# Performance work log

Hardware: AMD Instinct MI355X
Metric: run time of the kernel (lower is better)

Reference implementation:

```python
import jax, jax.numpy as jnp
import numpy as np

N_NODES = 50000
IN_CH, HID, OUT_CH = 512, 128, 64
N_EDGES = 800000


def gcn_conv(x, edge_index, W, b, num_nodes):
    # PyG GCNConv: add self-loops, symmetric deg^{-1/2} normalization,
    # linear transform then scatter-add aggregation at target nodes.
    row, col = edge_index[0], edge_index[1]
    loop = jnp.arange(num_nodes, dtype=row.dtype)
    rows = jnp.concatenate([row, loop])  # sources
    cols = jnp.concatenate([col, loop])  # targets
    deg = jax.ops.segment_sum(jnp.ones_like(cols, dtype=x.dtype), cols, num_segments=num_nodes)
    dinv = jnp.where(deg > 0, jax.lax.rsqrt(deg), 0.0)
    norm = dinv[rows] * dinv[cols]  # [E+N]
    h = x @ W  # [N, out]
    msg = norm[:, None] * h[rows]  # gather + scale
    out = jax.ops.segment_sum(msg, cols, num_segments=num_nodes)
    return out + b


def setup_inputs() -> dict:
    key = jax.random.key(0)
    k = jax.random.split(key, 8)
    x = jax.random.normal(k[0], (N_NODES, IN_CH), dtype=jnp.float32)
    pos_edge_index = jax.random.randint(k[1], (2, N_EDGES), 0, N_NODES, dtype=jnp.int64 if jax.config.jax_enable_x64 else jnp.int32)
    neg_edge_index = jax.random.randint(k[2], (2, N_EDGES), 0, N_NODES, dtype=pos_edge_index.dtype)
    # Glorot-ish init for weights, zeros for bias (PyG default)
    W1 = jax.random.normal(k[3], (IN_CH, HID), dtype=jnp.float32) * (1.0 / np.sqrt(IN_CH))
    b1 = jnp.zeros((HID,), dtype=jnp.float32)
    W2 = jax.random.normal(k[4], (HID, OUT_CH), dtype=jnp.float32) * (1.0 / np.sqrt(HID))
    b2 = jnp.zeros((OUT_CH,), dtype=jnp.float32)
    return {"x": x, "pos_edge_index": pos_edge_index, "neg_edge_index": neg_edge_index,
            "W1": W1, "b1": b1, "W2": W2, "b2": b2}


def reference(x, pos_edge_index, neg_edge_index, W1, b1, W2, b2):
    n = x.shape[0]
    h = gcn_conv(x, pos_edge_index, W1, b1, n)
    h = jax.nn.relu(h)
    z = gcn_conv(h, pos_edge_index, W2, b2, n)  # encode
    edge_index = jnp.concatenate([pos_edge_index, neg_edge_index], axis=-1)
    # decode: per-edge dot product of endpoint embeddings
    logits = jnp.sum(z[edge_index[0]] * z[edge_index[1]], axis=-1)
    return logits
```

## Files before the change

### kernel.cpp

```cpp
#include <hip/hip_runtime.h>

#define WAVE 64
#define CAP 64

typedef __bf16 v8bf __attribute__((ext_vector_type(8)));
typedef __bf16 v4bf __attribute__((ext_vector_type(4)));
typedef __bf16 v2bf __attribute__((ext_vector_type(2)));
typedef float f32x4 __attribute__((ext_vector_type(4)));

__device__ __forceinline__ void async16(void* lds, const void* g) {
    __builtin_amdgcn_global_load_lds((const __attribute__((address_space(1))) void*)g,
                                     (__attribute__((address_space(3))) void*)lds, 16, 0, 0);
}

__device__ __forceinline__ void cvt8(const f32x4& u, const f32x4& v, v8bf& h, v8bf& l) {
    float f[8] = {u.x, u.y, u.z, u.w, v.x, v.y, v.z, v.w};
#pragma unroll
    for (int j = 0; j < 8; ++j) {
        __bf16 hh = (__bf16)f[j];
        h[j] = hh;
        l[j] = (__bf16)(f[j] - (float)hh);
    }
}

__device__ __forceinline__ void cvt8f(const float4& u, const float4& v, v8bf& h, v8bf& l) {
    float f[8] = {u.x, u.y, u.z, u.w, v.x, v.y, v.z, v.w};
#pragma unroll
    for (int j = 0; j < 8; ++j) {
        __bf16 hh = (__bf16)f[j];
        h[j] = hh;
        l[j] = (__bf16)(f[j] - (float)hh);
    }
}

__global__ __launch_bounds__(256) void prep_kernel(const float* __restrict__ W1,
                                                   const float* __restrict__ W2,
                                                   __bf16* __restrict__ Wt1hi,
                                                   __bf16* __restrict__ Wt1lo,
                                                   __bf16* __restrict__ Wt2hi,
                                                   __bf16* __restrict__ Wt2lo) {
    int b = blockIdx.x;
    int tid = threadIdx.x;
    if (b < 256) {
        int idx = b * 256 + tid;
        int k = idx >> 7, n = idx & 127;
        float v = W1[idx];
        __bf16 h = (__bf16)v;
        Wt1hi[n * 512 + k] = h;
        Wt1lo[n * 512 + k] = (__bf16)(v - (float)h);
    } else {
        int idx = (b - 256) * 256 + tid;
        int k = idx >> 6, n = idx & 63;
        float v = W2[idx];
        __bf16 h = (__bf16)v;
        int o = (k >> 5) * (64 * 32) + n * 32 + (k & 31);
        Wt2hi[o] = h;
        Wt2lo[o] = (__bf16)(v - (float)h);
    }
}

__global__ __launch_bounds__(256) void fill_kernel(const int* __restrict__ ei, int E,
                                                   int* __restrict__ cursor,
                                                   unsigned short* __restrict__ srcs) {
    int e = blockIdx.x * 256 + (int)threadIdx.x;
    if (e >= E) return;
    int dst = ei[E + e];
    int src = ei[e];
    int p = atomicAdd(&cursor[dst], 1);
    if (p < CAP) srcs[(size_t)dst * CAP + p] = (unsigned short)src;
}

template <int NC, int KK, bool OBF16>
__global__ __launch_bounds__(256, 3) void gemm_dinv_kernel(
    const float* __restrict__ A, const __bf16* __restrict__ Bhi,
    const __bf16* __restrict__ Blo, void* __restrict__ Cout, int M, int NG,
    const int* __restrict__ cursor, float* __restrict__ dinv) {
    constexpr int BK = 32;
    constexpr int NT = NC / 16;
    constexpr int NIT = KK / BK;
    constexpr int NCH = NC / 16;

    __shared__ __bf16 sB[2][2][NC * BK];

    const int tid = threadIdx.x;

    if (blockIdx.x >= NG) {
        int i = (blockIdx.x - NG) * 256 + tid;
        if (i < M) dinv[i] = rsqrtf((float)cursor[i] + 1.0f);
        return;
    }

    const int lane = tid & 63;
    const int wv = tid >> 6;
    const int ln15 = lane & 15;
    const int quad = lane >> 4;
    const int rowBase = blockIdx.x * 128;

    const int brow = lane >> 2;
    const int bslot = lane & 3;
    auto stageB = [&](int buf, int k0) {
#pragma unroll
        for (int i = 0; i < NCH / 4; ++i) {
            int c = wv * (NCH / 4) + i;
            int row = c * 16 + brow;
            int gk = k0 + ((bslot ^ (row & 3)) << 3);
            async16(&sB[buf][0][c * 512], Bhi + (size_t)row * KK + gk);
            async16(&sB[buf][1][c * 512], Blo + (size_t)row * KK + gk);
        }
    };

    int r0 = rowBase + wv * 32 + ln15;
    int r1 = r0 + 16;
    if (r0 > M - 1) r0 = M - 1;
    if (r1 > M - 1) r1 = M - 1;
    const float* aP0 = A + (size_t)r0 * KK + quad * 8;
    const float* aP1 = A + (size_t)r1 * KK + quad * 8;

    f32x4 acc[2][NT];
#pragma unroll
    for (int rt = 0; rt < 2; ++rt)
#pragma unroll
        for (int t = 0; t < NT; ++t) acc[rt][t] = (f32x4){0.f, 0.f, 0.f, 0.f};

    float4 aR[4];
    aR[0] = *(const float4*)(aP0);
    aR[1] = *(const float4*)(aP0 + 4);
    aR[2] = *(const float4*)(aP1);
    aR[3] = *(const float4*)(aP1 + 4);

    stageB(0, 0);
    __syncthreads();

    int cur = 0;
    for (int ks = 0; ks < NIT; ++ks) {
        if (ks + 1 < NIT) stageB(cur ^ 1, (ks + 1) * BK);

        v8bf ah[2], al[2];
        cvt8f(aR[0], aR[1], ah[0], al[0]);
        cvt8f(aR[2], aR[3], ah[1], al[1]);
        if (ks + 1 < NIT) {
            aP0 += BK;
            aP1 += BK;
            aR[0] = *(const float4*)(aP0);
            aR[1] = *(const float4*)(aP0 + 4);
            aR[2] = *(const float4*)(aP1);
            aR[3] = *(const float4*)(aP1 + 4);
        }

#pragma unroll
        for (int t = 0; t < NT; ++t) {
            int row = t * 16 + ln15;
            int off = row * BK + ((quad ^ (row & 3)) << 3);
            v8bf bh = *(const v8bf*)&sB[cur][0][off];
            v8bf bl = *(const v8bf*)&sB[cur][1][off];
            acc[0][t] = __builtin_amdgcn_mfma_f32_16x16x32_bf16(ah[0], bh, acc[0][t], 0, 0, 0);
            acc[0][t] = __builtin_amdgcn_mfma_f32_16x16x32_bf16(al[0], bh, acc[0][t], 0, 0, 0);
            acc[0][t] = __builtin_amdgcn_mfma_f32_16x16x32_bf16(ah[0], bl, acc[0][t], 0, 0, 0);
            acc[1][t] = __builtin_amdgcn_mfma_f32_16x16x32_bf16(ah[1], bh, acc[1][t], 0, 0, 0);
            acc[1][t] = __builtin_amdgcn_mfma_f32_16x16x32_bf16(al[1], bh, acc[1][t], 0, 0, 0);
            acc[1][t] = __builtin_amdgcn_mfma_f32_16x16x32_bf16(ah[1], bl, acc[1][t], 0, 0, 0);
        }

        __syncthreads();
        cur ^= 1;
    }

#pragma unroll
    for (int rt = 0; rt < 2; ++rt) {
#pragma unroll
        for (int r = 0; r < 4; ++r) {
            int grow = rowBase + wv * 32 + rt * 16 + quad * 4 + r;
            if (grow < M) {
#pragma unroll
                for (int t = 0; t < NT; ++t) {
                    float v = acc[rt][t][r];
                    if (OBF16)
                        ((__bf16*)Cout)[(size_t)grow * NC + t * 16 + ln15] = (__bf16)v;
                    else
                        ((float*)Cout)[(size_t)grow * NC + t * 16 + ln15] = v;
                }
            }
        }
    }
}

__global__ __launch_bounds__(256) void gather1_gemm2_kernel(
    const __bf16* __restrict__ hs, const int* __restrict__ counts,
    const float* __restrict__ dinv, const unsigned short* __restrict__ srcs,
    const float* __restrict__ bias, const __bf16* __restrict__ W2hi,
    const __bf16* __restrict__ W2lo, __bf16* __restrict__ hs2, int N) {
    constexpr int LDO = 132;
    __shared__ float out1[16 * LDO];

    const int tid = threadIdx.x;
    const int lane = tid & 63;
    const int wv = tid >> 6;
    const int base = blockIdx.x * 16;

    for (int i = 0; i < 4; ++i) {
        int slot = wv * 4 + i;
        int node = base + slot;
        float v0 = 0.f, v1 = 0.f;
        int col = 2 * lane;
        if (node < N) {
            int cnt = counts[node];
            if (cnt > CAP) cnt = CAP;
            int beg = node * CAP;
            int end = beg + cnt;
            float dn = rsqrtf((float)cnt + 1.0f);
            float a0, a1;
            {
                v2bf s = *(const v2bf*)&hs[(size_t)node * 128 + col];
                a0 = dn * (float)s[0];
                a1 = dn * (float)s[1];
            }
            int e = beg;
            for (; e + 8 <= end; e += 8) {
                int s0 = srcs[e], s1 = srcs[e + 1], s2 = srcs[e + 2], s3 = srcs[e + 3];
                int s4 = srcs[e + 4], s5 = srcs[e + 5], s6 = srcs[e + 6], s7 = srcs[e + 7];
                float d0 = dinv[s0], d1 = dinv[s1], d2 = dinv[s2], d3 = dinv[s3];
                float d4 = dinv[s4], d5 = dinv[s5], d6 = dinv[s6], d7 = dinv[s7];
                v2bf r0 = *(const v2bf*)&hs[(size_t)s0 * 128 + col];
                v2bf r1 = *(const v2bf*)&hs[(size_t)s1 * 128 + col];
                v2bf r2 = *(const v2bf*)&hs[(size_t)s2 * 128 + col];
                v2bf r3 = *(const v2bf*)&hs[(size_t)s3 * 128 + col];
                v2bf r4 = *(const v2bf*)&hs[(size_t)s4 * 128 + col];
                v2bf r5 = *(const v2bf*)&hs[(size_t)s5 * 128 + col];
                v2bf r6 = *(const v2bf*)&hs[(size_t)s6 * 128 + col];
                v2bf r7 = *(const v2bf*)&hs[(size_t)s7 * 128 + col];
                a0 += d0 * (float)r0[0] + d1 * (float)r1[0] + d2 * (float)r2[0] + d3 * (float)r3[0] +
                      d4 * (float)r4[0] + d5 * (float)r5[0] + d6 * (float)r6[0] + d7 * (float)r7[0];
                a1 += d0 * (float)r0[1] + d1 * (float)r1[1] + d2 * (float)r2[1] + d3 * (float)r3[1] +
                      d4 * (float)r4[1] + d5 * (float)r5[1] + d6 * (float)r6[1] + d7 * (float)r7[1];
            }
            for (; e < end; ++e) {
                int s0 = srcs[e];
                float d0 = dinv[s0];
                v2bf r0 = *(const v2bf*)&hs[(size_t)s0 * 128 + col];
                a0 += d0 * (float)r0[0];
                a1 += d0 * (float)r0[1];
            }
            float2 bv = *(const float2*)&bias[col];
            v0 = fmaxf(dn * a0 + bv.x, 0.f);
            v1 = fmaxf(dn * a1 + bv.y, 0.f);
        }
        *(float2*)&out1[slot * LDO + col] = make_float2(v0, v1);
    }
    __syncthreads();

    const int ln15 = lane & 15;
    const int quad = lane >> 4;
    f32x4 acc = (f32x4){0.f, 0.f, 0.f, 0.f};
#pragma unroll
    for (int kc = 0; kc < 4; ++kc) {
        const float* ap = &out1[ln15 * LDO + kc * 32 + quad * 8];
        f32x4 u = *(const f32x4*)(ap);
        f32x4 v = *(const f32x4*)(ap + 4);
        v8bf ah, al;
        cvt8(u, v, ah, al);
        size_t bo = (size_t)kc * (64 * 32) + (wv * 16 + ln15) * 32 + quad * 8;
        v8bf bh = *(const v8bf*)(W2hi + bo);
        v8bf bl = *(const v8bf*)(W2lo + bo);
        acc = __builtin_amdgcn_mfma_f32_16x16x32_bf16(ah, bh, acc, 0, 0, 0);
        acc = __builtin_amdgcn_mfma_f32_16x16x32_bf16(al, bh, acc, 0, 0, 0);
        acc = __builtin_amdgcn_mfma_f32_16x16x32_bf16(ah, bl, acc, 0, 0, 0);
    }
#pragma unroll
    for (int r = 0; r < 4; ++r) {
        int node = base + quad * 4 + r;
        if (node < N) hs2[(size_t)node * 64 + wv * 16 + ln15] = (__bf16)acc[r];
    }
}

__global__ __launch_bounds__(256) void gather_agg2(const __bf16* __restrict__ hs,
                                                   const int* __restrict__ counts,
                                                   const float* __restrict__ dinv,
                                                   const unsigned short* __restrict__ srcs,
                                                   const float* __restrict__ bias,
                                                   __bf16* __restrict__ outp, int N) {
    int node = blockIdx.x * 4 + (int)(threadIdx.x >> 6);
    if (node >= N) return;
    int lane = threadIdx.x & 63;
    int cnt = counts[node];
    if (cnt > CAP) cnt = CAP;
    int beg = node * CAP;
    int end = beg + cnt;
    float dn = rsqrtf((float)cnt + 1.0f);

    int q = lane >> 4;
    int sl = lane & 15;
    int col = sl * 4;
    float a0 = 0.f, a1 = 0.f, a2 = 0.f, a3 = 0.f;
    if (q == 0) {
        v4bf s = *(const v4bf*)&hs[(size_t)node * 64 + col];
        a0 = dn * (float)s[0]; a1 = dn * (float)s[1];
        a2 = dn * (float)s[2]; a3 = dn * (float)s[3];
    }
    int e = beg + q;
    for (; e + 12 < end; e += 16) {
        int s0 = srcs[e], s1 = srcs[e + 4], s2 = srcs[e + 8], s3 = srcs[e + 12];
        float d0 = dinv[s0], d1 = dinv[s1], d2 = dinv[s2], d3 = dinv[s3];
        v4bf r0 = *(const v4bf*)&hs[(size_t)s0 * 64 + col];
        v4bf r1 = *(const v4bf*)&hs[(size_t)s1 * 64 + col];
        v4bf r2 = *(const v4bf*)&hs[(size_t)s2 * 64 + col];
        v4bf r3 = *(const v4bf*)&hs[(size_t)s3 * 64 + col];
        a0 += d0 * (float)r0[0] + d1 * (float)r1[0] + d2 * (float)r2[0] + d3 * (float)r3[0];
        a1 += d0 * (float)r0[1] + d1 * (float)r1[1] + d2 * (float)r2[1] + d3 * (float)r3[1];
        a2 += d0 * (float)r0[2] + d1 * (float)r1[2] + d2 * (float)r2[2] + d3 * (float)r3[2];
        a3 += d0 * (float)r0[3] + d1 * (float)r1[3] + d2 * (float)r2[3] + d3 * (float)r3[3];
    }
    for (; e < end; e += 4) {
        int s0 = srcs[e];
        float d0 = dinv[s0];
        v4bf r0 = *(const v4bf*)&hs[(size_t)s0 * 64 + col];
        a0 += d0 * (float)r0[0]; a1 += d0 * (float)r0[1];
        a2 += d0 * (float)r0[2]; a3 += d0 * (float)r0[3];
    }
    a0 += __shfl_xor(a0, 16); a0 += __shfl_xor(a0, 32);
    a1 += __shfl_xor(a1, 16); a1 += __shfl_xor(a1, 32);
    a2 += __shfl_xor(a2, 16); a2 += __shfl_xor(a2, 32);
    a3 += __shfl_xor(a3, 16); a3 += __shfl_xor(a3, 32);
    if (q == 0) {
        float4 bv = *(const float4*)&bias[col];
        v4bf o;
        o[0] = (__bf16)(dn * a0 + bv.x);
        o[1] = (__bf16)(dn * a1 + bv.y);
        o[2] = (__bf16)(dn * a2 + bv.z);
        o[3] = (__bf16)(dn * a3 + bv.w);
        *(v4bf*)&outp[(size_t)node * 64 + col] = o;
    }
}

__global__ __launch_bounds__(256) void decode_bf16_kernel(const __bf16* __restrict__ z,
                                                          const int* __restrict__ pos,
                                                          const int* __restrict__ neg, int E,
                                                          float* __restrict__ out) {
    int tid = blockIdx.x * blockDim.x + threadIdx.x;
    int g = tid >> 2;
    int l = tid & 3;
    int total = 2 * E;
    if (g >= total) return;
    int src, dst;
    if (g < E) {
        src = pos[g];
        dst = pos[E + g];
    } else {
        int e = g - E;
        src = neg[e];
        dst = neg[E + e];
    }
    const __bf16* zs = z + (size_t)src * 64 + l * 16;
    const __bf16* zd = z + (size_t)dst * 64 + l * 16;
    v8bf a0 = *(const v8bf*)zs;
    v8bf a1 = *(const v8bf*)(zs + 8);
    v8bf b0 = *(const v8bf*)zd;
    v8bf b1 = *(const v8bf*)(zd + 8);
    float p = 0.f;
#pragma unroll
    for (int j = 0; j < 8; ++j) p += (float)a0[j] * (float)b0[j] + (float)a1[j] * (float)b1[j];
    p += __shfl_xor(p, 1);
    p += __shfl_xor(p, 2);
    if (l == 0) out[g] = p;
}

extern "C" void kernel_launch(void* const* d_in, const int* in_sizes, int n_in, void* d_out,
                              int out_size, void* d_ws, size_t ws_size, hipStream_t stream) {
    const float* x = (const float*)d_in[0];
    const int* pos_ei = (const int*)d_in[1];
    const int* neg_ei = (const int*)d_in[2];
    const float* W1 = (const float*)d_in[3];
    const float* b1 = (const float*)d_in[4];
    const float* W2 = (const float*)d_in[5];
    const float* b2 = (const float*)d_in[6];
    float* out = (float*)d_out;

    const int IN = 512, HID = 128, OUT = 64;
    const int N = in_sizes[0] / IN;
    const int E = in_sizes[1] / 2;

    size_t nAlign = ((size_t)N + 255) & ~(size_t)255;
    float* p = (float*)d_ws;
    __bf16* hs1 = (__bf16*)p; p += (size_t)N * HID / 2;
    __bf16* hs2 = (__bf16*)p; p += (size_t)N * OUT / 2;
    __bf16* zbf = (__bf16*)p; p += (size_t)N * OUT / 2;
    int* cursor = (int*)p; p += nAlign;
    float* dinv = p; p += nAlign;
    unsigned short* srcs = (unsigned short*)p; p += (size_t)N * CAP / 2;
    __bf16* Wt1hi = (__bf16*)p; p += (size_t)IN * HID / 2;
    __bf16* Wt1lo = (__bf16*)p; p += (size_t)IN * HID / 2;
    __bf16* Wt2hi = (__bf16*)p; p += (size_t)HID * OUT / 2;
    __bf16* Wt2lo = (__bf16*)p; p += (size_t)HID * OUT / 2;

    const int NG = (N + 127) / 128;
    const int ND = (N + 255) / 256;

    hipMemsetAsync(cursor, 0, (size_t)N * sizeof(int), stream);
    prep_kernel<<<288, 256, 0, stream>>>(W1, W2, Wt1hi, Wt1lo, Wt2hi, Wt2lo);

    fill_kernel<<<(E + 255) / 256, 256, 0, stream>>>(pos_ei, E, cursor, srcs);

    gemm_dinv_kernel<128, 512, true><<<NG + ND, 256, 0, stream>>>(
        x, Wt1hi, Wt1lo, hs1, N, NG, cursor, dinv);

    gather1_gemm2_kernel<<<(N + 15) / 16, 256, 0, stream>>>(
        hs1, cursor, dinv, srcs, b1, Wt2hi, Wt2lo, hs2, N);

    gather_agg2<<<(N + 3) / 4, 256, 0, stream>>>(hs2, cursor, dinv, srcs, b2, zbf, N);

    decode_bf16_kernel<<<((size_t)2 * E * 4 + 255) / 256, 256, 0, stream>>>(
        zbf, pos_ei, neg_ei, E, out);
}
```

Measured before the change: 338.3 us.

## Fuse edge bucketing into layer-1 GEMM launch and pad per-node cursors

The standalone fill kernel is removed. Edge bucketing (atomic per-destination cursor plus source list) now runs in extra blocks of the layer-1 GEMM launch, so the atomic-heavy fill overlaps with the GEMM instead of running serially before it. dinv is computed in a new small kernel that runs after the GEMM. Each node's cursor is padded to 16 ints (64 bytes) so concurrent atomics on different nodes do not share cache lines. The cost is a 16x larger memset, strided count reads in the gather kernels, and one extra kernel launch.

Measured after the change: 315.5 us. 1.07x faster.

```diff
diff --git a/kernel.cpp b/kernel.cpp
--- a/kernel.cpp
+++ b/kernel.cpp
@@ -2,6 +2,7 @@
 
 #define WAVE 64
 #define CAP 64
+#define CURPAD 16
 
 typedef __bf16 v8bf __attribute__((ext_vector_type(8)));
 typedef __bf16 v4bf __attribute__((ext_vector_type(4)));
@@ -59,22 +60,12 @@
     }
 }
 
-__global__ __launch_bounds__(256) void fill_kernel(const int* __restrict__ ei, int E,
-                                                   int* __restrict__ cursor,
-                                                   unsigned short* __restrict__ srcs) {
-    int e = blockIdx.x * 256 + (int)threadIdx.x;
-    if (e >= E) return;
-    int dst = ei[E + e];
-    int src = ei[e];
-    int p = atomicAdd(&cursor[dst], 1);
-    if (p < CAP) srcs[(size_t)dst * CAP + p] = (unsigned short)src;
-}
-
 template <int NC, int KK, bool OBF16>
-__global__ __launch_bounds__(256, 3) void gemm_dinv_kernel(
+__global__ __launch_bounds__(256, 3) void gemm_fill_kernel(
     const float* __restrict__ A, const __bf16* __restrict__ Bhi,
     const __bf16* __restrict__ Blo, void* __restrict__ Cout, int M, int NG,
-    const int* __restrict__ cursor, float* __restrict__ dinv) {
+    const int* __restrict__ ei, int E, int* __restrict__ cursor,
+    unsigned short* __restrict__ srcs) {
     constexpr int BK = 32;
     constexpr int NT = NC / 16;
     constexpr int NIT = KK / BK;
@@ -85,8 +76,16 @@
     const int tid = threadIdx.x;
 
     if (blockIdx.x >= NG) {
-        int i = (blockIdx.x - NG) * 256 + tid;
-        if (i < M) dinv[i] = rsqrtf((float)cursor[i] + 1.0f);
+        int bb = (blockIdx.x - NG) * 512;
+#pragma unroll
+        for (int j = 0; j < 2; ++j) {
+            int e = bb + tid + j * 256;
+            if (e < E) {
+                int dst = ei[E + e];
+                int p = atomicAdd(&cursor[(size_t)dst * CURPAD], 1);
+                if (p < CAP) srcs[(size_t)dst * CAP + p] = (unsigned short)ei[e];
+            }
+        }
         return;
     }
 
@@ -184,6 +183,12 @@
     }
 }
 
+__global__ __launch_bounds__(256) void dinv_kernel(const int* __restrict__ cursor,
+                                                   float* __restrict__ dinv, int N) {
+    int i = blockIdx.x * 256 + (int)threadIdx.x;
+    if (i < N) dinv[i] = rsqrtf((float)cursor[(size_t)i * CURPAD] + 1.0f);
+}
+
 __global__ __launch_bounds__(256) void gather1_gemm2_kernel(
     const __bf16* __restrict__ hs, const int* __restrict__ counts,
     const float* __restrict__ dinv, const unsigned short* __restrict__ srcs,
@@ -203,7 +208,7 @@
         float v0 = 0.f, v1 = 0.f;
         int col = 2 * lane;
         if (node < N) {
-            int cnt = counts[node];
+            int cnt = counts[(size_t)node * CURPAD];
             if (cnt > CAP) cnt = CAP;
             int beg = node * CAP;
             int end = beg + cnt;
@@ -281,7 +286,7 @@
     int node = blockIdx.x * 4 + (int)(threadIdx.x >> 6);
     if (node >= N) return;
     int lane = threadIdx.x & 63;
-    int cnt = counts[node];
+    int cnt = counts[(size_t)node * CURPAD];
     if (cnt > CAP) cnt = CAP;
     int beg = node * CAP;
     int end = beg + cnt;
@@ -383,7 +388,7 @@
     __bf16* hs1 = (__bf16*)p; p += (size_t)N * HID / 2;
     __bf16* hs2 = (__bf16*)p; p += (size_t)N * OUT / 2;
     __bf16* zbf = (__bf16*)p; p += (size_t)N * OUT / 2;
-    int* cursor = (int*)p; p += nAlign;
+    int* cursor = (int*)p; p += nAlign * CURPAD;
     float* dinv = p; p += nAlign;
     unsigned short* srcs = (unsigned short*)p; p += (size_t)N * CAP / 2;
     __bf16* Wt1hi = (__bf16*)p; p += (size_t)IN * HID / 2;
@@ -392,15 +397,15 @@
     __bf16* Wt2lo = (__bf16*)p; p += (size_t)HID * OUT / 2;
 
     const int NG = (N + 127) / 128;
-    const int ND = (N + 255) / 256;
-
-    hipMemsetAsync(cursor, 0, (size_t)N * sizeof(int), stream);
+    const int NF = (E + 511) / 512;
+
+    hipMemsetAsync(cursor, 0, (size_t)N * CURPAD * sizeof(int), stream);
     prep_kernel<<<288, 256, 0, stream>>>(W1, W2, Wt1hi, Wt1lo, Wt2hi, Wt2lo);
 
-    fill_kernel<<<(E + 255) / 256, 256, 0, stream>>>(pos_ei, E, cursor, srcs);
-
-    gemm_dinv_kernel<128, 512, true><<<NG + ND, 256, 0, stream>>>(
-        x, Wt1hi, Wt1lo, hs1, N, NG, cursor, dinv);
+    gemm_fill_kernel<128, 512, true><<<NG + NF, 256, 0, stream>>>(
+        x, Wt1hi, Wt1lo, hs1, N, NG, pos_ei, E, cursor, srcs);
+
+    dinv_kernel<<<(N + 255) / 256, 256, 0, stream>>>(cursor, dinv, N);
 
     gather1_gemm2_kernel<<<(N + 15) / 16, 256, 0, stream>>>(
         hs1, cursor, dinv, srcs, b1, Wt2hi, Wt2lo, hs2, N);
```
